# Optimization experiments

Measured on AMD Instinct MI355X. Metric: run time of the kernel, lower is better.

Reference implementation:

```python
import jax, jax.numpy as jnp
import numpy as np
from jax import lax
from jax.scipy.special import logsumexp

NUM_BINS = 1001          # num_bins
K = 127                  # num_quantized_bins = 2**(8-1) - 1 (signed int8, non-narrow)
HALF = NUM_BINS // 2     # 500
EPS = 1e-4               # smoothing_eps
NEG = -1e30              # mask value for logsumexp


def setup_inputs() -> dict:
    key = jax.random.key(0)
    x = jax.random.normal(key, (8, 4096, 1024), dtype=jnp.float32)
    return {"x": x}


def _smooth_logits(v, valid, L):
    # Faithful to smooth_normalize_distribution: hist += eps*is_zeros - eps1*n_nonzeros
    is_zero = valid & (v == 0)
    n_zeros = jnp.sum(is_zero).astype(jnp.float32)
    n_nz = L.astype(jnp.float32) - n_zeros
    eps1 = EPS * n_zeros / jnp.maximum(n_nz, 1.0)
    logits = v + EPS * is_zero.astype(jnp.float32) - eps1 * n_nz
    return logits, n_nz


def reference(x):
    absmax = jnp.max(jnp.abs(x))
    edges = jnp.linspace(-absmax, absmax, NUM_BINS + 1)           # hist_edges, len 1002
    counts, _ = jnp.histogram(x.ravel(), bins=edges)
    hist = lax.stop_gradient(counts.astype(jnp.float32))          # torch.histc(...).int()
    csum = jnp.concatenate([jnp.zeros(1, jnp.float32), jnp.cumsum(hist)])  # exclusive prefix
    total = csum[-1]
    hist_pad = jnp.concatenate([hist, jnp.zeros(NUM_BINS, jnp.float32)])
    k = jnp.arange(NUM_BINS)

    def per_candidate(i):
        start = HALF - i
        stop = HALF + i + 1
        L = 2 * i + 1                          # length of sliced histogram
        valid = k < L
        sliced = lax.dynamic_slice(hist_pad, (start,), (NUM_BINS,))  # first L entries valid
        left = csum[start]                     # sum(hist[:start])
        right = total - csum[stop]             # sum(hist[stop:])
        p = sliced.at[0].add(left).at[L - 1].add(right)
        m = L // K                             # num_merged_bins
        seg = jnp.minimum(k // m, K - 1)       # merged-bin id per position (remainder -> last)
        seg_v = jnp.where(valid, seg, K)       # dump invalid into extra segment
        qb = jax.ops.segment_sum(jnp.where(valid, sliced, 0.0), seg_v, num_segments=K + 1)[:K]
        nz = valid & (sliced != 0)
        # norm for bin j counts nonzeros in its range; last bin uses stop=-1 (excludes k=L-1)
        cnt_mask = nz & (k != L - 1)
        norms = jax.ops.segment_sum(cnt_mask.astype(jnp.float32), seg_v, num_segments=K + 1)[:K]
        nk = norms[seg]
        qbk = qb[seg]
        # q[start:stop] = qb[j]/norm where norm != 0; k=L-1 never assigned; q[sliced==0]=0
        q = jnp.where(nz & (k != L - 1) & (nk > 0), qbk / jnp.maximum(nk, 1.0), 0.0)

        p_log, _ = _smooth_logits(p, valid, L)
        q_log, n_nz_q = _smooth_logits(q, valid, L)
        lZp = logsumexp(jnp.where(valid, p_log, NEG))
        lZq = logsumexp(jnp.where(valid, q_log, NEG))
        lp = p_log - lZp
        lq = q_log - lZq
        probs = jnp.where(valid, jnp.exp(lp), 0.0)
        kl = jnp.sum(probs * (lp - lq) * valid)
        kl = jnp.where(n_nz_q > 0, kl, jnp.inf)  # q all-zero -> divergence = inf
        return edges[stop], kl

    ivals = jnp.arange(K // 2, HALF + 1)        # i = 63 .. 500 (438 candidates)
    thresholds, divergence = jax.vmap(per_candidate)(ivals)
    return thresholds[jnp.argmin(divergence)]
```

## Files before the change

### kernel.cpp

```cpp
#include <hip/hip_runtime.h>
#include <math.h>

#define NBINS 1001
#define KQ 127
#define HALFB 500
#define SEPS 1e-4f
#define NCAND 438
#define IMIN 63
#define PMAXN 2048


static __device__ __forceinline__ float edge_at(int j, float stepv, float negabs) {
    return __fadd_rn(__fmul_rn((float)j, stepv), negabs);
}

static __device__ __forceinline__ void blockSum2(double& a, double& b, double* s8) {
    for (int s = 32; s > 0; s >>= 1) {
        a += __shfl_down(a, s, 64);
        b += __shfl_down(b, s, 64);
    }
    const int w = threadIdx.x >> 6, l = threadIdx.x & 63;
    __syncthreads();
    if (l == 0) { s8[w] = a; s8[4 + w] = b; }
    __syncthreads();
    a = (s8[0] + s8[1]) + (s8[2] + s8[3]);
    b = (s8[4] + s8[5]) + (s8[6] + s8[7]);
}

static __device__ __forceinline__ double blockSum1(double a, double* s8) {
    for (int s = 32; s > 0; s >>= 1) a += __shfl_down(a, s, 64);
    const int w = threadIdx.x >> 6, l = threadIdx.x & 63;
    __syncthreads();
    if (l == 0) s8[w] = a;
    __syncthreads();
    return (s8[0] + s8[1]) + (s8[2] + s8[3]);
}

static __device__ __forceinline__ void blockMax2(float& a, float& b, double* s8) {
    for (int s = 32; s > 0; s >>= 1) {
        a = fmaxf(a, __shfl_down(a, s, 64));
        b = fmaxf(b, __shfl_down(b, s, 64));
    }
    const int w = threadIdx.x >> 6, l = threadIdx.x & 63;
    __syncthreads();
    if (l == 0) { s8[w] = (double)a; s8[4 + w] = (double)b; }
    __syncthreads();
    a = fmaxf(fmaxf((float)s8[0], (float)s8[1]), fmaxf((float)s8[2], (float)s8[3]));
    b = fmaxf(fmaxf((float)s8[4], (float)s8[5]), fmaxf((float)s8[6], (float)s8[7]));
}


__global__ __launch_bounds__(256) void absmax_kernel(const float* __restrict__ x,
                                                     long long n,
                                                     float* __restrict__ pmax,
                                                     unsigned int* __restrict__ ws_u) {
    __shared__ float red[256];
    if (blockIdx.x == 0) {
        for (int t = threadIdx.x; t < NBINS; t += 256) ws_u[4 + t] = 0u;
        if (threadIdx.x == 0) ws_u[0] = 0u;
    }
    float m = 0.f;
    long long idx = (long long)blockIdx.x * blockDim.x + threadIdx.x;
    long long stride = (long long)gridDim.x * blockDim.x;
    const float4* x4 = (const float4*)x;
    long long n4 = n >> 2;
    long long i = idx;
    for (; i + stride < n4; i += 2 * stride) {
        float4 a = x4[i];
        float4 b = x4[i + stride];
        m = fmaxf(m, fmaxf(fmaxf(fabsf(a.x), fabsf(a.y)), fmaxf(fabsf(a.z), fabsf(a.w))));
        m = fmaxf(m, fmaxf(fmaxf(fabsf(b.x), fabsf(b.y)), fmaxf(fabsf(b.z), fabsf(b.w))));
    }
    for (; i < n4; i += stride) {
        float4 a = x4[i];
        m = fmaxf(m, fmaxf(fmaxf(fabsf(a.x), fabsf(a.y)), fmaxf(fabsf(a.z), fabsf(a.w))));
    }
    for (long long j = (n4 << 2) + idx; j < n; j += stride)
        m = fmaxf(m, fabsf(x[j]));
    red[threadIdx.x] = m;
    __syncthreads();
    for (int s = 128; s > 0; s >>= 1) {
        if (threadIdx.x < s) red[threadIdx.x] = fmaxf(red[threadIdx.x], red[threadIdx.x + s]);
        __syncthreads();
    }
    if (threadIdx.x == 0) pmax[blockIdx.x] = red[0];
}

static __device__ __forceinline__ void bin_one(float v, float inv, float cofs,
                                               float stepv, float negabs,
                                               unsigned int* __restrict__ sh) {
    float t = __builtin_fmaf(v, inv, cofs);
    int b = (int)t;
    b = b < 0 ? 0 : (b > NBINS - 1 ? NBINS - 1 : b);
    float e_lo = edge_at(b, stepv, negabs);
    float e_hi = edge_at(b + 1, stepv, negabs);
    int up = (v >= e_hi) & (b < NBINS - 1);
    int dn = (v < e_lo) & (b > 0);
    b += up - dn;
    unsigned int addr = (unsigned int)(unsigned long long)(&sh[b]);
    asm volatile("ds_add_u32 %0, %1" :: "v"(addr), "v"(1u));
}

__global__ __launch_bounds__(256) void hist_kernel(const float* __restrict__ x,
                                                   long long n,
                                                   const float* __restrict__ pmax,
                                                   unsigned int* __restrict__ hist,
                                                   unsigned int* __restrict__ absmax_bits) {
    __shared__ unsigned int sh[4 * NBINS];
    __shared__ float redm[256];
    {
        float m = 0.f;
        for (int t = threadIdx.x; t < PMAXN; t += 256) m = fmaxf(m, pmax[t]);
        redm[threadIdx.x] = m;
        __syncthreads();
        for (int s = 128; s > 0; s >>= 1) {
            if (threadIdx.x < s) redm[threadIdx.x] = fmaxf(redm[threadIdx.x], redm[threadIdx.x + s]);
            __syncthreads();
        }
    }
    float absmax = redm[0];
    if (blockIdx.x == 0 && threadIdx.x == 0) *absmax_bits = __float_as_uint(absmax);

    for (int i = threadIdx.x; i < 4 * NBINS; i += blockDim.x) sh[i] = 0u;
    __syncthreads();
    unsigned int* mysh = sh + (threadIdx.x >> 6) * NBINS;

    float negabs = -absmax;
    float stepv = __fdiv_rn(__fmul_rn(2.0f, absmax), 1001.0f);
    float inv = __fdiv_rn(1001.0f, __fmul_rn(2.0f, absmax));
    float cofs = __fmul_rn(absmax, inv);

    long long idx = (long long)blockIdx.x * blockDim.x + threadIdx.x;
    long long stride = (long long)gridDim.x * blockDim.x;
    const float4* x4 = (const float4*)x;
    long long n4 = n >> 2;
    long long i = idx;
    for (; i + stride < n4; i += 2 * stride) {
        float4 a = x4[i];
        float4 b = x4[i + stride];
        bin_one(a.x, inv, cofs, stepv, negabs, mysh);
        bin_one(a.y, inv, cofs, stepv, negabs, mysh);
        bin_one(a.z, inv, cofs, stepv, negabs, mysh);
        bin_one(a.w, inv, cofs, stepv, negabs, mysh);
        bin_one(b.x, inv, cofs, stepv, negabs, mysh);
        bin_one(b.y, inv, cofs, stepv, negabs, mysh);
        bin_one(b.z, inv, cofs, stepv, negabs, mysh);
        bin_one(b.w, inv, cofs, stepv, negabs, mysh);
    }
    for (; i < n4; i += stride) {
        float4 a = x4[i];
        bin_one(a.x, inv, cofs, stepv, negabs, mysh);
        bin_one(a.y, inv, cofs, stepv, negabs, mysh);
        bin_one(a.z, inv, cofs, stepv, negabs, mysh);
        bin_one(a.w, inv, cofs, stepv, negabs, mysh);
    }
    for (long long j = (n4 << 2) + idx; j < n; j += stride)
        bin_one(x[j], inv, cofs, stepv, negabs, mysh);

    asm volatile("s_waitcnt lgkmcnt(0)" ::: "memory");
    __syncthreads();
    for (int i2 = threadIdx.x; i2 < NBINS; i2 += blockDim.x) {
        unsigned int s = sh[i2] + sh[NBINS + i2] + sh[2 * NBINS + i2] + sh[3 * NBINS + i2];
        if (s) atomicAdd(&hist[i2], s);
    }
}

__global__ __launch_bounds__(1024) void scan_kernel(const unsigned int* __restrict__ hist,
                                                    double* __restrict__ csumD,
                                                    int* __restrict__ nzc) {
    __shared__ double sd[1024];
    __shared__ int si[1024];
    int t = threadIdx.x;
    unsigned int h = (t < NBINS) ? hist[t] : 0u;
    sd[t] = (double)((float)h);
    si[t] = (t < NBINS && h != 0u) ? 1 : 0;
    __syncthreads();
    for (int off = 1; off < 1024; off <<= 1) {
        double dv = 0.0; int iv = 0;
        if (t >= off) { dv = sd[t - off]; iv = si[t - off]; }
        __syncthreads();
        sd[t] += dv; si[t] += iv;
        __syncthreads();
    }
    if (t < NBINS) { csumD[t + 1] = sd[t]; nzc[t + 1] = si[t]; }
    if (t == 0) { csumD[0] = 0.0; nzc[0] = 0; }
}

__global__ __launch_bounds__(256) void cand_kernel(const unsigned int* __restrict__ hist,
                                                   const double* __restrict__ csumD,
                                                   const int* __restrict__ nzc,
                                                   float* __restrict__ divg) {
    const int i = IMIN + (int)blockIdx.x;
    const int L = 2 * i + 1;
    const int start = HALFB - i;
    const int stop = start + L;
    const int m = L / KQ;
    const unsigned int magic = (65536u + (unsigned)m - 1u) / (unsigned)m;
    const int tid = threadIdx.x;

    __shared__ float s_h[NBINS];
    __shared__ float s_qb[KQ];
    __shared__ float s_nkf[KQ];
    __shared__ double s8[8];

    for (int k = tid; k < NBINS; k += 256) s_h[k] = (float)hist[k];

    double csS = csumD[start], csE = csumD[stop], total = csumD[NBINS];
    float left = (float)csS;
    float right = (float)(total - csE);
    float s0 = (float)hist[start];
    float sL1 = (float)hist[stop - 1];
    int nzwin = nzc[stop] - nzc[start];
    int nnzq = nzwin - ((sL1 != 0.f) ? 1 : 0);
    int nzeros_s = L - nzwin;
    float n_zeros_p = (float)(nzeros_s
                              - ((s0 == 0.f && csS > 0.0) ? 1 : 0)
                              - ((sL1 == 0.f && (total - csE) > 0.0) ? 1 : 0));

    float n_nz_p = (float)L - n_zeros_p;
    float eps1p = SEPS * n_zeros_p / fmaxf(n_nz_p, 1.0f);
    float cp = eps1p * n_nz_p;

    float n_zeros_q = (float)L - (float)nnzq;
    float n_nz_qf = (float)L - n_zeros_q;
    float eps1q = SEPS * n_zeros_q / fmaxf(n_nz_qf, 1.0f);
    float cq = eps1q * n_nz_qf;

    if (tid < KQ) {
        int lo = start + tid * m;
        int hi = (tid == KQ - 1) ? stop : (lo + m);
        s_qb[tid] = (float)(csumD[hi] - csumD[lo]);
        int nrm = (nzc[hi] - nzc[lo]) - ((tid == KQ - 1 && sL1 != 0.f) ? 1 : 0);
        s_nkf[tid] = (float)nrm;
    }
    __syncthreads();

    float ppre[4], qpre[4];
    float maxpp = -INFINITY, maxqq = -INFINITY;
#pragma unroll
    for (int j = 0; j < 4; ++j) {
        int k = tid + 256 * j;
        ppre[j] = 0.f; qpre[j] = 0.f;
        if (k < L) {
            float s = s_h[start + k];
            float p = s;
            if (k == 0) p += left;
            if (k == L - 1) p += right;
            float pp = (p == 0.f) ? SEPS : p;
            int seg = (int)(((unsigned)k * magic) >> 16);
            if (seg > KQ - 1) seg = KQ - 1;
            float qv = 0.f;
            if (s != 0.f && k != L - 1) {
                float nk = s_nkf[seg];
                if (nk > 0.f) qv = s_qb[seg] / nk;
            }
            float qq = (qv == 0.f) ? SEPS : qv;
            ppre[j] = pp; qpre[j] = qq;
            maxpp = fmaxf(maxpp, pp);
            maxqq = fmaxf(maxqq, qq);
        }
    }
    blockMax2(maxpp, maxqq, s8);
    float maxplog = maxpp - cp;
    float maxqlog = maxqq - cq;

    double sp = 0.0, sq = 0.0;
#pragma unroll
    for (int j = 0; j < 4; ++j) {
        int k = tid + 256 * j;
        if (k < L) {
            sp += (double)expf((ppre[j] - cp) - maxplog);
            sq += (double)expf((qpre[j] - cq) - maxqlog);
        }
    }
    blockSum2(sp, sq, s8);
    float lZp = maxplog + (float)log(sp);
    float lZq = maxqlog + (float)log(sq);

    double kll = 0.0;
#pragma unroll
    for (int j = 0; j < 4; ++j) {
        int k = tid + 256 * j;
        if (k < L) {
            float pl = ppre[j] - cp;
            float ql = qpre[j] - cq;
            float lp = pl - lZp;
            float lq = ql - lZq;
            kll += (double)(expf(lp) * (lp - lq));
        }
    }
    double KL = blockSum1(kll, s8);
    if (tid == 0) divg[blockIdx.x] = (nnzq > 0) ? (float)KL : INFINITY;
}

__global__ void argmin_kernel(const float* __restrict__ divg,
                              const unsigned int* __restrict__ absmax_bits,
                              float* __restrict__ out) {
    __shared__ float vals[512];
    __shared__ int idxs[512];
    int tid = threadIdx.x;
    vals[tid] = (tid < NCAND) ? divg[tid] : INFINITY;
    idxs[tid] = tid;
    __syncthreads();
    for (int s = 256; s > 0; s >>= 1) {
        if (tid < s) {
            float a = vals[tid], b = vals[tid + s];
            int ia = idxs[tid], ib = idxs[tid + s];
            if (b < a || (b == a && ib < ia)) { vals[tid] = b; idxs[tid] = ib; }
        }
        __syncthreads();
    }
    if (tid == 0) {
        int i = IMIN + idxs[0];
        int stop = HALFB + i + 1;
        float absmax = __uint_as_float(*absmax_bits);
        float stepv = __fdiv_rn(__fmul_rn(2.0f, absmax), 1001.0f);
        out[0] = __fadd_rn(__fmul_rn((float)stop, stepv), -absmax);
    }
}

extern "C" void kernel_launch(void* const* d_in, const int* in_sizes, int n_in,
                              void* d_out, int out_size, void* d_ws, size_t ws_size,
                              hipStream_t stream) {
    const float* x = (const float*)d_in[0];
    long long n = (long long)in_sizes[0];

    unsigned int* ws_u = (unsigned int*)d_ws;
    unsigned int* absmax_bits = ws_u;
    unsigned int* hist = ws_u + 4;
    float* divg = (float*)(ws_u + 1028);
    double* csumD = (double*)(ws_u + 1536);
    int* nzc = (int*)(ws_u + 3544);
    float* pmax = (float*)(ws_u + 4608);
    float* out = (float*)d_out;

    hipLaunchKernelGGL(absmax_kernel, dim3(PMAXN), dim3(256), 0, stream, x, n, pmax, ws_u);
    hipLaunchKernelGGL(hist_kernel, dim3(1024), dim3(256), 0, stream, x, n, pmax, hist, absmax_bits);
    hipLaunchKernelGGL(scan_kernel, dim3(1), dim3(1024), 0, stream, hist, csumD, nzc);
    hipLaunchKernelGGL(cand_kernel, dim3(NCAND), dim3(256), 0, stream, hist, csumD, nzc, divg);
    hipLaunchKernelGGL(argmin_kernel, dim3(1), dim3(512), 0, stream, divg, absmax_bits, out);
}
```

Before: 245.6 us.

## Unroll streaming loops and fold argmin into candidate kernel via packed atomics

Both the absmax pass and the histogram pass now issue four float4 loads per iteration instead of two. The absmax pass also keeps four independent max accumulators, which gives more memory-level parallelism. The separate argmin kernel is removed: each candidate block does an atomicMin on a packed key made of the order-preserving KL bits and the block index. The last block to finish, found through an atomic counter, writes the threshold. This saves one kernel launch at the cost of extra register pressure in the streaming loops and reliance on correct atomic ordering.

```diff
diff --git a/kernel.cpp b/kernel.cpp
--- a/kernel.cpp
+++ b/kernel.cpp
@@ -57,26 +57,35 @@
     __shared__ float red[256];
     if (blockIdx.x == 0) {
         for (int t = threadIdx.x; t < NBINS; t += 256) ws_u[4 + t] = 0u;
-        if (threadIdx.x == 0) ws_u[0] = 0u;
-    }
-    float m = 0.f;
+        if (threadIdx.x == 0) {
+            ws_u[0] = 0u;
+            ws_u[1008] = 0u;
+            *(unsigned long long*)(ws_u + 2) = ~0ULL;
+        }
+    }
+    float m0 = 0.f, m1 = 0.f, m2 = 0.f, m3 = 0.f;
     long long idx = (long long)blockIdx.x * blockDim.x + threadIdx.x;
     long long stride = (long long)gridDim.x * blockDim.x;
     const float4* x4 = (const float4*)x;
     long long n4 = n >> 2;
     long long i = idx;
-    for (; i + stride < n4; i += 2 * stride) {
+    for (; i + 3 * stride < n4; i += 4 * stride) {
         float4 a = x4[i];
         float4 b = x4[i + stride];
-        m = fmaxf(m, fmaxf(fmaxf(fabsf(a.x), fabsf(a.y)), fmaxf(fabsf(a.z), fabsf(a.w))));
-        m = fmaxf(m, fmaxf(fmaxf(fabsf(b.x), fabsf(b.y)), fmaxf(fabsf(b.z), fabsf(b.w))));
+        float4 c = x4[i + 2 * stride];
+        float4 d = x4[i + 3 * stride];
+        m0 = fmaxf(m0, fmaxf(fmaxf(fabsf(a.x), fabsf(a.y)), fmaxf(fabsf(a.z), fabsf(a.w))));
+        m1 = fmaxf(m1, fmaxf(fmaxf(fabsf(b.x), fabsf(b.y)), fmaxf(fabsf(b.z), fabsf(b.w))));
+        m2 = fmaxf(m2, fmaxf(fmaxf(fabsf(c.x), fabsf(c.y)), fmaxf(fabsf(c.z), fabsf(c.w))));
+        m3 = fmaxf(m3, fmaxf(fmaxf(fabsf(d.x), fabsf(d.y)), fmaxf(fabsf(d.z), fabsf(d.w))));
     }
     for (; i < n4; i += stride) {
         float4 a = x4[i];
-        m = fmaxf(m, fmaxf(fmaxf(fabsf(a.x), fabsf(a.y)), fmaxf(fabsf(a.z), fabsf(a.w))));
+        m0 = fmaxf(m0, fmaxf(fmaxf(fabsf(a.x), fabsf(a.y)), fmaxf(fabsf(a.z), fabsf(a.w))));
     }
     for (long long j = (n4 << 2) + idx; j < n; j += stride)
-        m = fmaxf(m, fabsf(x[j]));
+        m0 = fmaxf(m0, fabsf(x[j]));
+    float m = fmaxf(fmaxf(m0, m1), fmaxf(m2, m3));
     red[threadIdx.x] = m;
     __syncthreads();
     for (int s = 128; s > 0; s >>= 1) {
@@ -135,9 +144,11 @@
     const float4* x4 = (const float4*)x;
     long long n4 = n >> 2;
     long long i = idx;
-    for (; i + stride < n4; i += 2 * stride) {
+    for (; i + 3 * stride < n4; i += 4 * stride) {
         float4 a = x4[i];
         float4 b = x4[i + stride];
+        float4 c = x4[i + 2 * stride];
+        float4 d = x4[i + 3 * stride];
         bin_one(a.x, inv, cofs, stepv, negabs, mysh);
         bin_one(a.y, inv, cofs, stepv, negabs, mysh);
         bin_one(a.z, inv, cofs, stepv, negabs, mysh);
@@ -146,6 +157,14 @@
         bin_one(b.y, inv, cofs, stepv, negabs, mysh);
         bin_one(b.z, inv, cofs, stepv, negabs, mysh);
         bin_one(b.w, inv, cofs, stepv, negabs, mysh);
+        bin_one(c.x, inv, cofs, stepv, negabs, mysh);
+        bin_one(c.y, inv, cofs, stepv, negabs, mysh);
+        bin_one(c.z, inv, cofs, stepv, negabs, mysh);
+        bin_one(c.w, inv, cofs, stepv, negabs, mysh);
+        bin_one(d.x, inv, cofs, stepv, negabs, mysh);
+        bin_one(d.y, inv, cofs, stepv, negabs, mysh);
+        bin_one(d.z, inv, cofs, stepv, negabs, mysh);
+        bin_one(d.w, inv, cofs, stepv, negabs, mysh);
     }
     for (; i < n4; i += stride) {
         float4 a = x4[i];
@@ -189,7 +208,8 @@
 __global__ __launch_bounds__(256) void cand_kernel(const unsigned int* __restrict__ hist,
                                                    const double* __restrict__ csumD,
                                                    const int* __restrict__ nzc,
-                                                   float* __restrict__ divg) {
+                                                   unsigned int* __restrict__ ws_u,
+                                                   float* __restrict__ out) {
     const int i = IMIN + (int)blockIdx.x;
     const int L = 2 * i + 1;
     const int start = HALFB - i;
@@ -290,32 +310,25 @@
         }
     }
     double KL = blockSum1(kll, s8);
-    if (tid == 0) divg[blockIdx.x] = (nnzq > 0) ? (float)KL : INFINITY;
-}
-
-__global__ void argmin_kernel(const float* __restrict__ divg,
-                              const unsigned int* __restrict__ absmax_bits,
-                              float* __restrict__ out) {
-    __shared__ float vals[512];
-    __shared__ int idxs[512];
-    int tid = threadIdx.x;
-    vals[tid] = (tid < NCAND) ? divg[tid] : INFINITY;
-    idxs[tid] = tid;
-    __syncthreads();
-    for (int s = 256; s > 0; s >>= 1) {
-        if (tid < s) {
-            float a = vals[tid], b = vals[tid + s];
-            int ia = idxs[tid], ib = idxs[tid + s];
-            if (b < a || (b == a && ib < ia)) { vals[tid] = b; idxs[tid] = ib; }
-        }
-        __syncthreads();
-    }
+
     if (tid == 0) {
-        int i = IMIN + idxs[0];
-        int stop = HALFB + i + 1;
-        float absmax = __uint_as_float(*absmax_bits);
-        float stepv = __fdiv_rn(__fmul_rn(2.0f, absmax), 1001.0f);
-        out[0] = __fadd_rn(__fmul_rn((float)stop, stepv), -absmax);
+        float kl = (nnzq > 0) ? (float)KL : INFINITY;
+        unsigned int u = __float_as_uint(kl);
+        u = (u & 0x80000000u) ? ~u : (u | 0x80000000u);
+        unsigned long long key = ((unsigned long long)u << 16) | (unsigned int)blockIdx.x;
+        unsigned long long* packed = (unsigned long long*)(ws_u + 2);
+        atomicMin(packed, key);
+        __threadfence();
+        unsigned int prev = atomicAdd(&ws_u[1008], 1u);
+        if (prev == NCAND - 1) {
+            unsigned long long win = atomicAdd(packed, 0ULL);
+            int widx = (int)(win & 0xFFFFull);
+            int wi = IMIN + widx;
+            int wstop = HALFB + wi + 1;
+            float absmax = __uint_as_float(ws_u[0]);
+            float stepv = __fdiv_rn(__fmul_rn(2.0f, absmax), 1001.0f);
+            out[0] = __fadd_rn(__fmul_rn((float)wstop, stepv), -absmax);
+        }
     }
 }
 
@@ -328,7 +341,6 @@
     unsigned int* ws_u = (unsigned int*)d_ws;
     unsigned int* absmax_bits = ws_u;
     unsigned int* hist = ws_u + 4;
-    float* divg = (float*)(ws_u + 1028);
     double* csumD = (double*)(ws_u + 1536);
     int* nzc = (int*)(ws_u + 3544);
     float* pmax = (float*)(ws_u + 4608);
@@ -337,6 +349,5 @@
     hipLaunchKernelGGL(absmax_kernel, dim3(PMAXN), dim3(256), 0, stream, x, n, pmax, ws_u);
     hipLaunchKernelGGL(hist_kernel, dim3(1024), dim3(256), 0, stream, x, n, pmax, hist, absmax_bits);
     hipLaunchKernelGGL(scan_kernel, dim3(1), dim3(1024), 0, stream, hist, csumD, nzc);
-    hipLaunchKernelGGL(cand_kernel, dim3(NCAND), dim3(256), 0, stream, hist, csumD, nzc, divg);
-    hipLaunchKernelGGL(argmin_kernel, dim3(1), dim3(512), 0, stream, divg, absmax_bits, out);
-}
+    hipLaunchKernelGGL(cand_kernel, dim3(NCAND), dim3(256), 0, stream, hist, csumD, nzc, ws_u, out);
+}
```

Result: no change. 250.3 us (+1.9%).
